# Performance work log

Hardware: AMD Instinct MI355X
Metric: run time of the kernel (lower is better)

Reference implementation:

```python
import jax, jax.numpy as jnp
import numpy as np

N = 2048
D_T = 256; D_F = 256
E_T = 32; E_F = 32; E_C = 128
C = 5; Q = 512


def setup_inputs() -> dict:
    key = jax.random.key(0)
    ks = jax.random.split(key, 12)
    # full graph minus self-loops, row-major (matches dense_to_sparse ordering)
    r, c = np.meshgrid(np.arange(N), np.arange(N), indexing='ij')
    m = r != c
    edge_index = jnp.asarray(np.stack([r[m], c[m]]), dtype=jnp.int32)  # [2, N*(N-1)]
    E = edge_index.shape[1]
    s = 0.02
    return {
        'time_features': jax.random.normal(ks[0], (N, D_T), jnp.float32),
        'edge_index': edge_index,
        'time_edge_weight': jax.random.uniform(ks[1], (E,), jnp.float32),
        'freq_features': jax.random.normal(ks[2], (N, D_F), jnp.float32),
        'freq_edge_weight': jax.random.uniform(ks[3], (E,), jnp.float32),
        'labels': jax.random.randint(ks[4], (N,), 0, C, jnp.int32),
        'num_classes': C,
        'query_size': Q,
        'Wt': jax.random.normal(ks[5], (D_T, E_T), jnp.float32) * s,
        'bt': jnp.zeros((E_T,), jnp.float32),
        'Wf': jax.random.normal(ks[6], (D_F, E_F), jnp.float32) * s,
        'bf': jnp.zeros((E_F,), jnp.float32),
        'Wc': jax.random.normal(ks[7], (E_T + E_F + C, E_C), jnp.float32) * s,
        'bc': jnp.zeros((E_C,), jnp.float32),
        'Wo': jax.random.normal(ks[8], (E_C, C), jnp.float32) * s,
        'bo': jnp.zeros((C,), jnp.float32),
    }


def _gcn(x, A, W, b):
    # torch_geometric GCNConv: D^{-1/2}(A + I)D^{-1/2} (X W) + b
    n = A.shape[0]
    Ah = A + jnp.eye(n, dtype=A.dtype)
    deg = Ah.sum(axis=1)
    dis = jnp.where(deg > 0, jax.lax.rsqrt(deg), 0.0)
    return (dis[:, None] * Ah * dis[None, :]) @ (x @ W) + b


def reference(time_features, edge_index, time_edge_weight, freq_features,
              freq_edge_weight, labels, num_classes, query_size,
              Wt, bt, Wf, bf, Wc, bc, Wo, bo):
    n = time_features.shape[0]
    lrelu = lambda z: jax.nn.leaky_relu(z, 0.01)

    def dense_adj(w):  # A[dst, src] = w
        return jnp.zeros((n, n), w.dtype).at[edge_index[1], edge_index[0]].add(w)

    te = lrelu(_gcn(time_features, dense_adj(time_edge_weight), Wt, bt))
    fe = lrelu(_gcn(freq_features, dense_adj(freq_edge_weight), Wf, bf))

    # to_one_hot: one_hot[:n - query_size, labels] = 1 -> support rows get 1 in
    # every column that appears anywhere in `labels`
    cols = jnp.zeros((num_classes,), te.dtype).at[labels].set(1.0)
    rowmask = (jnp.arange(n) < (n - query_size)).astype(te.dtype)
    one_hot = rowmask[:, None] * cols[None, :]

    feats = jnp.concatenate([te, fe, one_hot], axis=-1)  # [n, E_T+E_F+C]

    # graph_construction (no_grad in original): 1 / (L1 distance over the
    # non-one-hot dims + 1e-5), zero diagonal
    fd = jax.lax.stop_gradient(feats[:, : feats.shape[1] - num_classes])
    dist = jnp.sum(jnp.abs(fd[:, None, :] - fd[None, :, :]), axis=-1)  # [n, n]
    Aw = (1.0 / (dist + 1e-5)) * (1.0 - jnp.eye(n, dtype=feats.dtype))

    emb = lrelu(_gcn(feats, Aw, Wc, bc))
    return emb @ Wo + bo
```

## Files before the change

kernel.cpp:

```cpp
#include <hip/hip_runtime.h>
#include <hip/hip_bf16.h>

#define N 2048
#define NM1 2047
#define DT 256
#define ET 32
#define EC 128
#define NC 5
#define FS 80
#define FD 69
#define KC_ET 16
#define KC_EC 16

typedef unsigned short u16;
typedef unsigned int u32;
typedef float f32x4 __attribute__((ext_vector_type(4)));
typedef __bf16 bf16x8 __attribute__((ext_vector_type(8)));

__device__ inline u16 bf16_rne(float x){
    unsigned int b = __float_as_uint(x);
    b += 0x7fffu + ((b >> 16) & 1u);
    return (u16)(b >> 16);
}
__device__ inline float bf16_to_f(u16 h){
    return __uint_as_float(((unsigned int)h) << 16);
}
__device__ inline f32x4 mfma16x16x32(bf16x8 a, bf16x8 b, f32x4 c){
    return __builtin_amdgcn_mfma_f32_16x16x32_bf16(a, b, c, 0, 0, 0);
}

__global__ __launch_bounds__(256) void k_deg_label_xw(const float* __restrict__ tw,
                                                      const float* __restrict__ fw,
                                                      const int* __restrict__ labels,
                                                      const float* __restrict__ Xt,
                                                      const float* __restrict__ Wt,
                                                      const float* __restrict__ Xf,
                                                      const float* __restrict__ Wf,
                                                      float* __restrict__ degT,
                                                      float* __restrict__ degF,
                                                      float* __restrict__ cols,
                                                      float* __restrict__ Yt,
                                                      float* __restrict__ Yf){
    int b = blockIdx.x;
    int t = threadIdx.x;
    if (b < 512){
        int p = (b & 7)*256 + t;
        if (p >= NM1) return;
        int s0 = (b >> 3)*32;
        float lowT=0.f, highT=0.f, lowF=0.f, highF=0.f;
        #pragma unroll 8
        for (int r = 0; r < 32; ++r){
            int s = s0 + r;
            float vt = tw[(size_t)s*NM1 + p];
            float vf = fw[(size_t)s*NM1 + p];
            if (s <= p){ highT += vt; highF += vf; }
            else       { lowT  += vt; lowF  += vf; }
        }
        atomicAdd(&degT[p],   lowT);
        atomicAdd(&degF[p],   lowF);
        atomicAdd(&degT[p+1], highT);
        atomicAdd(&degF[p+1], highF);
        return;
    }
    if (b == 512){
        __shared__ float lc[NC];
        if (t < NC) lc[t] = 0.f;
        __syncthreads();
        for (int i = t; i < N; i += 256){
            int l = labels[i];
            if (l >= 0 && l < NC) lc[l] = 1.f;
        }
        __syncthreads();
        if (t < NC) cols[t] = lc[t];
        return;
    }
    int idx = b - 513;
    const float* X = (idx & 256) ? Xf : Xt;
    const float* W = (idx & 256) ? Wf : Wt;
    float*       Y = (idx & 256) ? Yf : Yt;
    __shared__ float Ws[DT*ET];
    __shared__ float Xs[8*DT];
    for (int j = t; j < DT*ET; j += 256) Ws[j] = W[j];
    int i0 = (idx & 255)*8;
    for (int j = t; j < 8*DT; j += 256) Xs[j] = X[(size_t)i0*DT + j];
    __syncthreads();
    int r = t >> 5, f = t & 31;
    const float* xr = Xs + r*DT;
    float acc = 0.f;
    #pragma unroll 8
    for (int d = 0; d < DT; ++d) acc += xr[d]*Ws[d*ET+f];
    Y[(size_t)(i0+r)*ET+f] = acc;
}

__global__ __launch_bounds__(256) void k_agg_et_m(const float* __restrict__ tw,
                                                  const float* __restrict__ fw,
                                                  const float* __restrict__ Yt,
                                                  const float* __restrict__ Yf,
                                                  const float* __restrict__ degT,
                                                  const float* __restrict__ degF,
                                                  float* __restrict__ Pt,
                                                  float* __restrict__ Pf){
    __shared__ u16 Zs[2][2][32][136];
    int t = threadIdx.x;
    int w = t >> 6, l = t & 63, lr = l & 15, lg = l >> 4;
    int g = w >> 1, wh = w & 1;
    int i0 = blockIdx.x*32;
    int kc = blockIdx.y;
    int k0 = kc*128;

    {
        int f = t >> 3;
        int kb16 = (t & 7)*16;
        #pragma unroll
        for (int gg = 0; gg < 2; ++gg){
            const float* Y   = gg ? Yf   : Yt;
            const float* deg = gg ? degF : degT;
            u16 h8[16], l8[16];
            #pragma unroll
            for (int j = 0; j < 16; ++j){
                int k = k0 + kb16 + j;
                float rd = rsqrtf(1.f + deg[k]);
                float v = rd * Y[(size_t)k*ET + f];
                u16 h = bf16_rne(v);
                h8[j] = h;
                l8[j] = bf16_rne(v - bf16_to_f(h));
            }
            uint4 pk;
            pk.x = (u32)h8[0] | ((u32)h8[1]<<16);
            pk.y = (u32)h8[2] | ((u32)h8[3]<<16);
            pk.z = (u32)h8[4] | ((u32)h8[5]<<16);
            pk.w = (u32)h8[6] | ((u32)h8[7]<<16);
            *(uint4*)&Zs[gg][0][f][kb16] = pk;
            pk.x = (u32)h8[8]  | ((u32)h8[9]<<16);
            pk.y = (u32)h8[10] | ((u32)h8[11]<<16);
            pk.z = (u32)h8[12] | ((u32)h8[13]<<16);
            pk.w = (u32)h8[14] | ((u32)h8[15]<<16);
            *(uint4*)&Zs[gg][0][f][kb16+8] = pk;
            pk.x = (u32)l8[0] | ((u32)l8[1]<<16);
            pk.y = (u32)l8[2] | ((u32)l8[3]<<16);
            pk.z = (u32)l8[4] | ((u32)l8[5]<<16);
            pk.w = (u32)l8[6] | ((u32)l8[7]<<16);
            *(uint4*)&Zs[gg][1][f][kb16] = pk;
            pk.x = (u32)l8[8]  | ((u32)l8[9]<<16);
            pk.y = (u32)l8[10] | ((u32)l8[11]<<16);
            pk.z = (u32)l8[12] | ((u32)l8[13]<<16);
            pk.w = (u32)l8[14] | ((u32)l8[15]<<16);
            *(uint4*)&Zs[gg][1][f][kb16+8] = pk;
        }
    }
    __syncthreads();

    const float* A = g ? fw : tw;
    f32x4 acc[2];
    acc[0] = (f32x4){0.f,0.f,0.f,0.f};
    acc[1] = (f32x4){0.f,0.f,0.f,0.f};

    for (int sub = 0; sub < 2; ++sub){
        int kb = k0 + sub*64;
        int row = i0 + wh*16 + lr;
        #pragma unroll
        for (int ks = 0; ks < 2; ++ks){
            int kbase = kb + ks*32 + lg*8;
            u16 ah[8], al[8];
            #pragma unroll
            for (int j = 0; j < 8; ++j){
                int k = kbase + j;
                float v = 0.f;
                if (row != k) v = A[(size_t)k*NM1 + row - (row > k ? 1 : 0)];
                u16 h = bf16_rne(v);
                ah[j] = h;
                al[j] = bf16_rne(v - bf16_to_f(h));
            }
            uint4 pa, pb;
            pa.x = (u32)ah[0] | ((u32)ah[1]<<16);
            pa.y = (u32)ah[2] | ((u32)ah[3]<<16);
            pa.z = (u32)ah[4] | ((u32)ah[5]<<16);
            pa.w = (u32)ah[6] | ((u32)ah[7]<<16);
            pb.x = (u32)al[0] | ((u32)al[1]<<16);
            pb.y = (u32)al[2] | ((u32)al[3]<<16);
            pb.z = (u32)al[4] | ((u32)al[5]<<16);
            pb.w = (u32)al[6] | ((u32)al[7]<<16);
            bf16x8 aH = *(bf16x8*)&pa;
            bf16x8 aL = *(bf16x8*)&pb;
            int koff = sub*64 + ks*32 + lg*8;
            #pragma unroll
            for (int ff = 0; ff < 2; ++ff){
                bf16x8 bH = *(const bf16x8*)&Zs[g][0][ff*16+lr][koff];
                bf16x8 bL = *(const bf16x8*)&Zs[g][1][ff*16+lr][koff];
                acc[ff] = mfma16x16x32(aH, bH, acc[ff]);
                acc[ff] = mfma16x16x32(aL, bH, acc[ff]);
                acc[ff] = mfma16x16x32(aH, bL, acc[ff]);
            }
        }
    }
    float* P = g ? Pf : Pt;
    #pragma unroll
    for (int ff = 0; ff < 2; ++ff)
        #pragma unroll
        for (int r = 0; r < 4; ++r){
            int gi = i0 + wh*16 + lg*4 + r;
            P[(size_t)kc*(N*ET) + (size_t)gi*ET + ff*16 + lr] = acc[ff][r];
        }
}

__global__ __launch_bounds__(256) void k_feats_epi(const float* __restrict__ Pt,
                                                   const float* __restrict__ Pf,
                                                   const float* __restrict__ Yt,
                                                   const float* __restrict__ Yf,
                                                   const float* __restrict__ degT,
                                                   const float* __restrict__ degF,
                                                   const float* __restrict__ bt,
                                                   const float* __restrict__ bfv,
                                                   const float* __restrict__ cols,
                                                   const int* __restrict__ qsize,
                                                   float* __restrict__ feats){
    int idx = blockIdx.x*256 + threadIdx.x;
    int i = idx >> 6;
    int f = idx & 63;
    float s, rd, b;
    if (f < ET){
        rd = rsqrtf(1.f + degT[i]);
        s = rd*Yt[(size_t)i*ET + f];
        #pragma unroll
        for (int kc = 0; kc < KC_ET; ++kc) s += Pt[(size_t)kc*(N*ET) + (size_t)i*ET + f];
        b = bt[f];
    } else {
        int g = f - ET;
        rd = rsqrtf(1.f + degF[i]);
        s = rd*Yf[(size_t)i*ET + g];
        #pragma unroll
        for (int kc = 0; kc < KC_ET; ++kc) s += Pf[(size_t)kc*(N*ET) + (size_t)i*ET + g];
        b = bfv[g];
    }
    float v = rd*s + b;
    feats[(size_t)i*FS + f] = v > 0.f ? v : 0.01f*v;
    if (f < NC){
        int nsup = N - qsize[0];
        feats[(size_t)i*FS + 2*ET + f] = (i < nsup) ? cols[f] : 0.f;
    }
}

__global__ __launch_bounds__(256) void k_aw_zc(const float* __restrict__ feats,
                                               const float* __restrict__ Wc,
                                               u16* __restrict__ Aw_hi,
                                               u16* __restrict__ Aw_lo,
                                               u16* __restrict__ ZcT_hi,
                                               u16* __restrict__ ZcT_lo,
                                               float* __restrict__ dsum){
    __shared__ __align__(16) char sm[37632];
    int t = threadIdx.x;
    int b = blockIdx.x;
    if (b < 1024){
        float* fiT = (float*)sm;
        float* fjT = fiT + 64*68;
        int i0 = (b & 31)*64, j0 = (b >> 5)*64;
        {
            int row = t >> 2;
            int cb  = (t & 3)*16;
            const float4* si = (const float4*)(feats + (size_t)(i0+row)*FS + cb);
            const float4* sj = (const float4*)(feats + (size_t)(j0+row)*FS + cb);
            #pragma unroll
            for (int s = 0; s < 4; ++s){
                float4 v = si[s];
                float4 w = sj[s];
                int c = cb + s*4;
                fiT[(c+0)*68+row]=v.x; fiT[(c+1)*68+row]=v.y; fiT[(c+2)*68+row]=v.z; fiT[(c+3)*68+row]=v.w;
                fjT[(c+0)*68+row]=w.x; fjT[(c+1)*68+row]=w.y; fjT[(c+2)*68+row]=w.z; fjT[(c+3)*68+row]=w.w;
            }
        }
        __syncthreads();
        int tx = t & 15, ty = t >> 4;
        float acc[4][4];
        #pragma unroll
        for (int u=0;u<4;++u)
            #pragma unroll
            for (int v=0;v<4;++v) acc[u][v]=0.f;
        for (int d = 0; d < 64; ++d){
            float4 a4 = *(const float4*)&fiT[d*68 + ty*4];
            float4 b4 = *(const float4*)&fjT[d*68 + tx*4];
            const float* ap = (const float*)&a4;
            const float* bp = (const float*)&b4;
            #pragma unroll
            for (int u = 0; u < 4; ++u)
                #pragma unroll
                for (int v = 0; v < 4; ++v)
                    acc[u][v] += fabsf(ap[u]-bp[v]);
        }
        #pragma unroll
        for (int u = 0; u < 4; ++u){
            int gi = i0 + ty*4 + u;
            float po[4];
            u16 hh[4], ll[4];
            #pragma unroll
            for (int v = 0; v < 4; ++v){
                int gj = j0 + tx*4 + v;
                float w = (gi==gj) ? 1.0f : 1.0f/(acc[u][v] + 1e-5f);
                po[v] = w;
                u16 h = bf16_rne(w);
                hh[v] = h;
                ll[v] = bf16_rne(w - bf16_to_f(h));
            }
            uint2 ph, pl;
            ph.x = (u32)hh[0] | ((u32)hh[1]<<16);
            ph.y = (u32)hh[2] | ((u32)hh[3]<<16);
            pl.x = (u32)ll[0] | ((u32)ll[1]<<16);
            pl.y = (u32)ll[2] | ((u32)ll[3]<<16);
            *(uint2*)&Aw_hi[(size_t)gi*N + j0 + tx*4] = ph;
            *(uint2*)&Aw_lo[(size_t)gi*N + j0 + tx*4] = pl;
            float rs = (po[0]+po[1]) + (po[2]+po[3]);
            rs += __shfl_xor(rs, 1);
            rs += __shfl_xor(rs, 2);
            rs += __shfl_xor(rs, 4);
            rs += __shfl_xor(rs, 8);
            if (tx == 0) atomicAdd(&dsum[gi], rs);
        }
        return;
    }
    {
        float* Wcs = (float*)sm;
        float* fr  = Wcs + FD*EC;
        int idx = b - 1024;
        int i0 = idx*8;
        for (int j = t; j < FD*EC; j += 256) Wcs[j] = Wc[j];
        for (int j = t; j < 8*FD; j += 256){
            int r = j / FD;
            int c = j - r*FD;
            fr[r*72 + c] = feats[(size_t)(i0+r)*FS + c];
        }
        __syncthreads();
        int f  = t & 127;
        int rh = t >> 7;
        u16 hh[4], ll[4];
        #pragma unroll
        for (int rr = 0; rr < 4; ++rr){
            int r = rh*4 + rr;
            float acc = 0.f;
            #pragma unroll
            for (int d = 0; d < FD; ++d) acc += fr[r*72+d]*Wcs[d*EC+f];
            u16 h = bf16_rne(acc);
            hh[rr] = h;
            ll[rr] = bf16_rne(acc - bf16_to_f(h));
        }
        uint2 ph, pl;
        ph.x = (u32)hh[0] | ((u32)hh[1]<<16);
        ph.y = (u32)hh[2] | ((u32)hh[3]<<16);
        pl.x = (u32)ll[0] | ((u32)ll[1]<<16);
        pl.y = (u32)ll[2] | ((u32)ll[3]<<16);
        *(uint2*)&ZcT_hi[(size_t)f*N + i0 + rh*4] = ph;
        *(uint2*)&ZcT_lo[(size_t)f*N + i0 + rh*4] = pl;
    }
}

__global__ __launch_bounds__(256) void k_agg_ec(const u16* __restrict__ Aw_hi,
                                                const u16* __restrict__ Aw_lo,
                                                const u16* __restrict__ ZcT_hi,
                                                const u16* __restrict__ ZcT_lo,
                                                const float* __restrict__ dsum,
                                                float* __restrict__ Pe){
    __shared__ u16 Ah[64*72];
    __shared__ u16 Al[64*72];
    __shared__ u16 Zh[64*72];
    __shared__ u16 Zl[64*72];
    int t = threadIdx.x;
    int w  = t >> 6;
    int l  = t & 63;
    int lr = l & 15;
    int lg = l >> 4;
    int i0 = (blockIdx.x >> 1)*64;
    int fh = blockIdx.x & 1;
    int kb0 = blockIdx.y*128;
    f32x4 acc[4];
    #pragma unroll
    for (int tt = 0; tt < 4; ++tt) acc[tt] = (f32x4){0.f, 0.f, 0.f, 0.f};

    for (int sub = 0; sub < 2; ++sub){
        int kbs = kb0 + sub*64;
        #pragma unroll
        for (int e = 0; e < 2; ++e){
            int id = t + e*256;
            int row = id >> 3, ch = (id & 7)*8;
            uint4 vh = *(const uint4*)&Aw_hi[(size_t)(i0+row)*N + kbs + ch];
            uint4 vl = *(const uint4*)&Aw_lo[(size_t)(i0+row)*N + kbs + ch];
            const u16* ph = (const u16*)&vh;
            const u16* pl = (const u16*)&vl;
            u16 nh[8], nl[8];
            #pragma unroll
            for (int j = 0; j < 8; ++j){
                float a = bf16_to_f(ph[j]) + bf16_to_f(pl[j]);
                float v = a * rsqrtf(dsum[kbs + ch + j]);
                u16 h = bf16_rne(v);
                nh[j] = h;
                nl[j] = bf16_rne(v - bf16_to_f(h));
            }
            uint4 oh, ol;
            oh.x = (u32)nh[0] | ((u32)nh[1]<<16);
            oh.y = (u32)nh[2] | ((u32)nh[3]<<16);
            oh.z = (u32)nh[4] | ((u32)nh[5]<<16);
            oh.w = (u32)nh[6] | ((u32)nh[7]<<16);
            ol.x = (u32)nl[0] | ((u32)nl[1]<<16);
            ol.y = (u32)nl[2] | ((u32)nl[3]<<16);
            ol.z = (u32)nl[4] | ((u32)nl[5]<<16);
            ol.w = (u32)nl[6] | ((u32)nl[7]<<16);
            *(uint4*)&Ah[row*72 + ch] = oh;
            *(uint4*)&Al[row*72 + ch] = ol;
        }
        #pragma unroll
        for (int e = 0; e < 2; ++e){
            int id = t + e*256;
            int row = id >> 3, ch = (id & 7)*8;
            uint4 vh = *(const uint4*)&ZcT_hi[(size_t)(fh*64 + row)*N + kbs + ch];
            uint4 vl = *(const uint4*)&ZcT_lo[(size_t)(fh*64 + row)*N + kbs + ch];
            *(uint4*)&Zh[row*72 + ch] = vh;
            *(uint4*)&Zl[row*72 + ch] = vl;
        }
        __syncthreads();
        #pragma unroll
        for (int ks = 0; ks < 2; ++ks){
            int aoff = (w*16 + lr)*72 + ks*32 + lg*8;
            bf16x8 aH = *(const bf16x8*)&Ah[aoff];
            bf16x8 aL = *(const bf16x8*)&Al[aoff];
            #pragma unroll
            for (int tt = 0; tt < 4; ++tt){
                int zoff = (tt*16 + lr)*72 + ks*32 + lg*8;
                bf16x8 bH = *(const bf16x8*)&Zh[zoff];
                bf16x8 bL = *(const bf16x8*)&Zl[zoff];
                acc[tt] = mfma16x16x32(aH, bH, acc[tt]);
                acc[tt] = mfma16x16x32(aL, bH, acc[tt]);
                acc[tt] = mfma16x16x32(aH, bL, acc[tt]);
            }
        }
        __syncthreads();
    }
    #pragma unroll
    for (int tt = 0; tt < 4; ++tt){
        #pragma unroll
        for (int r = 0; r < 4; ++r){
            int gi = i0 + w*16 + lg*4 + r;
            Pe[(size_t)blockIdx.y*(N*EC) + (size_t)gi*EC + fh*64 + tt*16 + lr] = acc[tt][r];
        }
    }
}

__global__ __launch_bounds__(256) void k_embfinal(const float* __restrict__ Pe,
                                                  const float* __restrict__ dsum,
                                                  const float* __restrict__ bc,
                                                  const float* __restrict__ Wo,
                                                  const float* __restrict__ bo,
                                                  float* __restrict__ out){
    __shared__ float vs[2][EC];
    __shared__ float Wos[EC*NC];
    __shared__ float bos[NC];
    int t = threadIdx.x;
    for (int idx = t; idx < EC*NC; idx += 256) Wos[idx] = Wo[idx];
    if (t < NC) bos[t] = bo[t];
    int rr = t >> 7, f = t & 127;
    int i = blockIdx.x*2 + rr;
    size_t idx = (size_t)i*EC + f;
    float s = 0.f;
    #pragma unroll
    for (int kc = 0; kc < KC_EC; ++kc) s += Pe[(size_t)kc*(N*EC) + idx];
    float v = rsqrtf(dsum[i])*s + bc[f];
    vs[rr][f] = v > 0.f ? v : 0.01f*v;
    __syncthreads();
    if (t < 2*NC){
        int r = t / NC;
        int c = t - r*NC;
        float a = bos[c];
        #pragma unroll 8
        for (int f2 = 0; f2 < EC; ++f2) a += vs[r][f2]*Wos[f2*NC+c];
        out[(size_t)(blockIdx.x*2 + r)*NC + c] = a;
    }
}

extern "C" void kernel_launch(void* const* d_in, const int* in_sizes, int n_in,
                              void* d_out, int out_size, void* d_ws, size_t ws_size,
                              hipStream_t stream) {
    const float* time_features = (const float*)d_in[0];
    const float* tw            = (const float*)d_in[2];
    const float* freq_features = (const float*)d_in[3];
    const float* fw            = (const float*)d_in[4];
    const int*   labels        = (const int*)d_in[5];
    const int*   qsize         = (const int*)d_in[7];
    const float* Wt  = (const float*)d_in[8];
    const float* bt  = (const float*)d_in[9];
    const float* Wf  = (const float*)d_in[10];
    const float* bfv = (const float*)d_in[11];
    const float* Wc  = (const float*)d_in[12];
    const float* bc  = (const float*)d_in[13];
    const float* Wo  = (const float*)d_in[14];
    const float* bo  = (const float*)d_in[15];
    float* out = (float*)d_out;

    float* ws    = (float*)d_ws;
    float* degT  = ws;
    float* degF  = degT + N;
    float* dsum  = degF + N;
    float* colsb = dsum + N;
    float* Yt    = colsb + 8;
    float* Yf    = Yt + (size_t)N*ET;
    float* feats = Yf + (size_t)N*ET;
    float* Zc    = feats + (size_t)N*FS;
    float* Aw    = Zc + (size_t)N*EC;
    float* Pt    = Aw + (size_t)N*N;
    float* Pf    = Pt + (size_t)KC_ET*N*ET;
    float* Pe    = Pf + (size_t)KC_ET*N*ET;

    u16* ZcT_hi = (u16*)Zc;
    u16* ZcT_lo = ZcT_hi + (size_t)N*EC;
    u16* Aw_hi  = (u16*)Aw;
    u16* Aw_lo  = Aw_hi + (size_t)N*N;

    hipMemsetAsync(degT, 0, 3*N*sizeof(float), stream);
    k_deg_label_xw<<<1025, 256, 0, stream>>>(tw, fw, labels,
                                             time_features, Wt, freq_features, Wf,
                                             degT, degF, colsb, Yt, Yf);
    k_agg_et_m<<<dim3(N/32, KC_ET), 256, 0, stream>>>(tw, fw, Yt, Yf, degT, degF, Pt, Pf);
    k_feats_epi<<<(N*64)/256, 256, 0, stream>>>(Pt, Pf, Yt, Yf, degT, degF,
                                                bt, bfv, colsb, qsize, feats);
    k_aw_zc<<<1280, 256, 0, stream>>>(feats, Wc, Aw_hi, Aw_lo, ZcT_hi, ZcT_lo, dsum);
    k_agg_ec<<<dim3(64, KC_EC), 256, 0, stream>>>(Aw_hi, Aw_lo, ZcT_hi, ZcT_lo, dsum, Pe);
    k_embfinal<<<N/2, 256, 0, stream>>>(Pe, dsum, bc, Wo, bo, out);
}
```

Before: 196.7 us.

## Enlarge output tiles in both aggregation kernels to reuse staged operands

The time/frequency aggregation kernel now handles 64 rows per block instead of 32, so each block reuses the staged, degree-scaled Z tile in shared memory across twice as many rows. The Aw aggregation kernel now computes all 128 output features per block instead of splitting them into two halves. That means each Aw hi/lo tile, including its normalization work, is loaded and converted once instead of twice. The cost is fewer blocks (halved grids), more accumulator registers, and twice the shared memory for the Z tile, all of which can lower occupancy.

```diff
diff --git a/kernel.cpp b/kernel.cpp
--- a/kernel.cpp
+++ b/kernel.cpp
@@ -104,7 +104,7 @@
     int t = threadIdx.x;
     int w = t >> 6, l = t & 63, lr = l & 15, lg = l >> 4;
     int g = w >> 1, wh = w & 1;
-    int i0 = blockIdx.x*32;
+    int i0 = blockIdx.x*64;
     int kc = blockIdx.y;
     int k0 = kc*128;
 
@@ -151,56 +151,63 @@
     __syncthreads();
 
     const float* A = g ? fw : tw;
-    f32x4 acc[2];
-    acc[0] = (f32x4){0.f,0.f,0.f,0.f};
-    acc[1] = (f32x4){0.f,0.f,0.f,0.f};
+    f32x4 acc[2][2];
+    #pragma unroll
+    for (int fi = 0; fi < 2; ++fi)
+        #pragma unroll
+        for (int ff = 0; ff < 2; ++ff) acc[fi][ff] = (f32x4){0.f,0.f,0.f,0.f};
 
     for (int sub = 0; sub < 2; ++sub){
         int kb = k0 + sub*64;
-        int row = i0 + wh*16 + lr;
-        #pragma unroll
-        for (int ks = 0; ks < 2; ++ks){
-            int kbase = kb + ks*32 + lg*8;
-            u16 ah[8], al[8];
-            #pragma unroll
-            for (int j = 0; j < 8; ++j){
-                int k = kbase + j;
-                float v = 0.f;
-                if (row != k) v = A[(size_t)k*NM1 + row - (row > k ? 1 : 0)];
-                u16 h = bf16_rne(v);
-                ah[j] = h;
-                al[j] = bf16_rne(v - bf16_to_f(h));
-            }
-            uint4 pa, pb;
-            pa.x = (u32)ah[0] | ((u32)ah[1]<<16);
-            pa.y = (u32)ah[2] | ((u32)ah[3]<<16);
-            pa.z = (u32)ah[4] | ((u32)ah[5]<<16);
-            pa.w = (u32)ah[6] | ((u32)ah[7]<<16);
-            pb.x = (u32)al[0] | ((u32)al[1]<<16);
-            pb.y = (u32)al[2] | ((u32)al[3]<<16);
-            pb.z = (u32)al[4] | ((u32)al[5]<<16);
-            pb.w = (u32)al[6] | ((u32)al[7]<<16);
-            bf16x8 aH = *(bf16x8*)&pa;
-            bf16x8 aL = *(bf16x8*)&pb;
-            int koff = sub*64 + ks*32 + lg*8;
-            #pragma unroll
-            for (int ff = 0; ff < 2; ++ff){
-                bf16x8 bH = *(const bf16x8*)&Zs[g][0][ff*16+lr][koff];
-                bf16x8 bL = *(const bf16x8*)&Zs[g][1][ff*16+lr][koff];
-                acc[ff] = mfma16x16x32(aH, bH, acc[ff]);
-                acc[ff] = mfma16x16x32(aL, bH, acc[ff]);
-                acc[ff] = mfma16x16x32(aH, bL, acc[ff]);
+        #pragma unroll
+        for (int fi = 0; fi < 2; ++fi){
+            int row = i0 + wh*32 + fi*16 + lr;
+            #pragma unroll
+            for (int ks = 0; ks < 2; ++ks){
+                int kbase = kb + ks*32 + lg*8;
+                u16 ah[8], al[8];
+                #pragma unroll
+                for (int j = 0; j < 8; ++j){
+                    int k = kbase + j;
+                    float v = 0.f;
+                    if (row != k) v = A[(size_t)k*NM1 + row - (row > k ? 1 : 0)];
+                    u16 h = bf16_rne(v);
+                    ah[j] = h;
+                    al[j] = bf16_rne(v - bf16_to_f(h));
+                }
+                uint4 pa, pb;
+                pa.x = (u32)ah[0] | ((u32)ah[1]<<16);
+                pa.y = (u32)ah[2] | ((u32)ah[3]<<16);
+                pa.z = (u32)ah[4] | ((u32)ah[5]<<16);
+                pa.w = (u32)ah[6] | ((u32)ah[7]<<16);
+                pb.x = (u32)al[0] | ((u32)al[1]<<16);
+                pb.y = (u32)al[2] | ((u32)al[3]<<16);
+                pb.z = (u32)al[4] | ((u32)al[5]<<16);
+                pb.w = (u32)al[6] | ((u32)al[7]<<16);
+                bf16x8 aH = *(bf16x8*)&pa;
+                bf16x8 aL = *(bf16x8*)&pb;
+                int koff = sub*64 + ks*32 + lg*8;
+                #pragma unroll
+                for (int ff = 0; ff < 2; ++ff){
+                    bf16x8 bH = *(const bf16x8*)&Zs[g][0][ff*16+lr][koff];
+                    bf16x8 bL = *(const bf16x8*)&Zs[g][1][ff*16+lr][koff];
+                    acc[fi][ff] = mfma16x16x32(aH, bH, acc[fi][ff]);
+                    acc[fi][ff] = mfma16x16x32(aL, bH, acc[fi][ff]);
+                    acc[fi][ff] = mfma16x16x32(aH, bL, acc[fi][ff]);
+                }
             }
         }
     }
     float* P = g ? Pf : Pt;
     #pragma unroll
-    for (int ff = 0; ff < 2; ++ff)
-        #pragma unroll
-        for (int r = 0; r < 4; ++r){
-            int gi = i0 + wh*16 + lg*4 + r;
-            P[(size_t)kc*(N*ET) + (size_t)gi*ET + ff*16 + lr] = acc[ff][r];
-        }
+    for (int fi = 0; fi < 2; ++fi)
+        #pragma unroll
+        for (int ff = 0; ff < 2; ++ff)
+            #pragma unroll
+            for (int r = 0; r < 4; ++r){
+                int gi = i0 + wh*32 + fi*16 + lg*4 + r;
+                P[(size_t)kc*(N*ET) + (size_t)gi*ET + ff*16 + lr] = acc[fi][ff][r];
+            }
 }
 
 __global__ __launch_bounds__(256) void k_feats_epi(const float* __restrict__ Pt,
@@ -359,19 +366,18 @@
                                                 float* __restrict__ Pe){
     __shared__ u16 Ah[64*72];
     __shared__ u16 Al[64*72];
-    __shared__ u16 Zh[64*72];
-    __shared__ u16 Zl[64*72];
+    __shared__ u16 Zh[128*72];
+    __shared__ u16 Zl[128*72];
     int t = threadIdx.x;
     int w  = t >> 6;
     int l  = t & 63;
     int lr = l & 15;
     int lg = l >> 4;
-    int i0 = (blockIdx.x >> 1)*64;
-    int fh = blockIdx.x & 1;
+    int i0 = blockIdx.x*64;
     int kb0 = blockIdx.y*128;
-    f32x4 acc[4];
+    f32x4 acc[8];
     #pragma unroll
-    for (int tt = 0; tt < 4; ++tt) acc[tt] = (f32x4){0.f, 0.f, 0.f, 0.f};
+    for (int tt = 0; tt < 8; ++tt) acc[tt] = (f32x4){0.f, 0.f, 0.f, 0.f};
 
     for (int sub = 0; sub < 2; ++sub){
         int kbs = kb0 + sub*64;
@@ -405,11 +411,11 @@
             *(uint4*)&Al[row*72 + ch] = ol;
         }
         #pragma unroll
-        for (int e = 0; e < 2; ++e){
+        for (int e = 0; e < 4; ++e){
             int id = t + e*256;
             int row = id >> 3, ch = (id & 7)*8;
-            uint4 vh = *(const uint4*)&ZcT_hi[(size_t)(fh*64 + row)*N + kbs + ch];
-            uint4 vl = *(const uint4*)&ZcT_lo[(size_t)(fh*64 + row)*N + kbs + ch];
+            uint4 vh = *(const uint4*)&ZcT_hi[(size_t)row*N + kbs + ch];
+            uint4 vl = *(const uint4*)&ZcT_lo[(size_t)row*N + kbs + ch];
             *(uint4*)&Zh[row*72 + ch] = vh;
             *(uint4*)&Zl[row*72 + ch] = vl;
         }
@@ -420,7 +426,7 @@
             bf16x8 aH = *(const bf16x8*)&Ah[aoff];
             bf16x8 aL = *(const bf16x8*)&Al[aoff];
             #pragma unroll
-            for (int tt = 0; tt < 4; ++tt){
+            for (int tt = 0; tt < 8; ++tt){
                 int zoff = (tt*16 + lr)*72 + ks*32 + lg*8;
                 bf16x8 bH = *(const bf16x8*)&Zh[zoff];
                 bf16x8 bL = *(const bf16x8*)&Zl[zoff];
@@ -432,11 +438,11 @@
         __syncthreads();
     }
     #pragma unroll
-    for (int tt = 0; tt < 4; ++tt){
+    for (int tt = 0; tt < 8; ++tt){
         #pragma unroll
         for (int r = 0; r < 4; ++r){
             int gi = i0 + w*16 + lg*4 + r;
-            Pe[(size_t)blockIdx.y*(N*EC) + (size_t)gi*EC + fh*64 + tt*16 + lr] = acc[tt][r];
+            Pe[(size_t)blockIdx.y*(N*EC) + (size_t)gi*EC + tt*16 + lr] = acc[tt][r];
         }
     }
 }
@@ -514,10 +520,10 @@
     k_deg_label_xw<<<1025, 256, 0, stream>>>(tw, fw, labels,
                                              time_features, Wt, freq_features, Wf,
                                              degT, degF, colsb, Yt, Yf);
-    k_agg_et_m<<<dim3(N/32, KC_ET), 256, 0, stream>>>(tw, fw, Yt, Yf, degT, degF, Pt, Pf);
+    k_agg_et_m<<<dim3(N/64, KC_ET), 256, 0, stream>>>(tw, fw, Yt, Yf, degT, degF, Pt, Pf);
     k_feats_epi<<<(N*64)/256, 256, 0, stream>>>(Pt, Pf, Yt, Yf, degT, degF,
                                                 bt, bfv, colsb, qsize, feats);
     k_aw_zc<<<1280, 256, 0, stream>>>(feats, Wc, Aw_hi, Aw_lo, ZcT_hi, ZcT_lo, dsum);
-    k_agg_ec<<<dim3(64, KC_EC), 256, 0, stream>>>(Aw_hi, Aw_lo, ZcT_hi, ZcT_lo, dsum, Pe);
+    k_agg_ec<<<dim3(N/64, KC_EC), 256, 0, stream>>>(Aw_hi, Aw_lo, ZcT_hi, ZcT_lo, dsum, Pe);
     k_embfinal<<<N/2, 256, 0, stream>>>(Pe, dsum, bc, Wo, bo, out);
 }
```

Result: faster. 192.7 us (-2.1%).
